# Performance work log

Hardware: AMD Instinct MI355X
Metric: run time of the kernel (lower is better)

Reference implementation:

```python
import jax, jax.numpy as jnp
import numpy as np

MARGIN = 0.2  # init margin
B, D = 4096, 512


def _pairwise_dist(x):
    # torch.cdist(x, x, p=2): Euclidean distance via Gram matrix
    sq = jnp.sum(x * x, axis=-1)                      # [B]
    gram = x @ x.T                                    # [B, B]
    d2 = jnp.maximum(sq[:, None] + sq[None, :] - 2.0 * gram, 0.0)
    safe = jnp.where(d2 > 0, d2, 1.0)                 # grad-safe sqrt at 0
    return jnp.where(d2 > 0, jnp.sqrt(safe), 0.0)


def setup_inputs() -> dict:
    key = jax.random.key(0)
    k1, k2, k3 = jax.random.split(key, 3)
    anchor = jax.random.normal(k1, (B, D), dtype=jnp.float32)
    positive = jax.random.normal(k2, (B, D), dtype=jnp.float32)
    labels = jax.random.randint(k3, (B,), 0, 64)
    return {"anchor": anchor, "positive": positive, "labels": labels}


def reference(anchor, positive, labels):
    d_ap = jnp.sum((anchor - positive) ** 2, axis=-1)          # [B] squared dist
    pd = _pairwise_dist(anchor)                                 # [B, B] euclidean
    diff_label = labels[None, :] != labels[:, None]             # [B, B]
    inf = jnp.float32(jnp.inf)
    # negatives farther than the positive (note: pd is euclidean, d_ap squared,
    # exactly as in the original code)
    cand = jnp.where(diff_label & (pd > d_ap[:, None]), pd, inf)
    min_larger = jnp.min(cand, axis=1)
    # fallback: min over all different-label negatives
    fallback = jnp.min(jnp.where(diff_label, pd, inf), axis=1)
    d_an = jnp.where(jnp.isfinite(min_larger), min_larger, fallback)
    loss = jnp.maximum(d_ap - d_an + MARGIN, 0.0)
    return jnp.mean(loss)
```

## Files before the change

kernel.cpp:

```cpp
#include <hip/hip_runtime.h>
#include <hip/hip_bf16.h>
#include <cstdint>
#include <cstddef>

constexpr int BN = 4096;
constexpr int DN = 512;
constexpr int NT = BN / 128;
constexpr int NBLK = NT * (NT + 1) / 2;
constexpr float MARGIN = 0.2f;
constexpr uint32_t INF_U = 0x7f800000u;

typedef __attribute__((ext_vector_type(8))) short short8;
typedef __attribute__((ext_vector_type(4))) float float4v;

__global__ __launch_bounds__(256) void prep_kernel(
    const float* __restrict__ anchor,
    const float* __restrict__ positive,
    const int* __restrict__ labels,
    uint16_t* __restrict__ Abf,
    float4* __restrict__ meta,
    uint32_t* __restrict__ min_all,
    uint32_t* __restrict__ min_larger,
    uint32_t* __restrict__ done_count)
{
    const int tid  = threadIdx.x;
    const int wave = tid >> 6;
    const int lane = tid & 63;
    const int row  = blockIdx.x * 4 + wave;

    if (blockIdx.x == 0 && tid == 0) *done_count = 0;

    const float4* arow = (const float4*)(anchor   + (size_t)row * DN);
    const float4* prow = (const float4*)(positive + (size_t)row * DN);

    float4 av0 = arow[lane * 2 + 0], av1 = arow[lane * 2 + 1];
    float4 pv0 = prow[lane * 2 + 0], pv1 = prow[lane * 2 + 1];

    float a[8] = {av0.x, av0.y, av0.z, av0.w, av1.x, av1.y, av1.z, av1.w};
    float p[8] = {pv0.x, pv0.y, pv0.z, pv0.w, pv1.x, pv1.y, pv1.z, pv1.w};

    float s = 0.f, d = 0.f;
    union { uint16_t u[8]; uint4 v; } pk;
    #pragma unroll
    for (int i = 0; i < 8; ++i) {
        s += a[i] * a[i];
        float dx = a[i] - p[i];
        d += dx * dx;
        uint32_t ub = __float_as_uint(a[i]);
        pk.u[i] = (uint16_t)((ub + 0x7fffu + ((ub >> 16) & 1u)) >> 16);
    }

    ((uint4*)(Abf + (size_t)row * DN))[lane] = pk.v;

    #pragma unroll
    for (int off = 32; off; off >>= 1) {
        s += __shfl_xor(s, off);
        d += __shfl_xor(d, off);
    }
    if (lane == 0) {
        meta[row] = (float4){s, d, d * d, __uint_as_float((uint32_t)labels[row])};
        min_all[row]    = INF_U;
        min_larger[row] = INF_U;
    }
}

__global__ __launch_bounds__(256, 2) void gram_kernel(
    const uint16_t* __restrict__ Abf,
    const float4* __restrict__ meta,
    uint32_t* __restrict__ min_all,
    uint32_t* __restrict__ min_larger,
    uint32_t* __restrict__ done_count,
    float* __restrict__ out)
{
    __shared__ uint16_t Abuf[128 * 128];
    __shared__ uint16_t Bbuf[128 * 128];

    int t = blockIdx.x, bi = 0, rem = NT;
    while (t >= rem) { t -= rem; ++bi; --rem; }
    const int bj = bi + t;
    const bool offdiag = (bi != bj);
    const int rowBase = bi * 128;
    const int colBase = bj * 128;

    const int tid  = threadIdx.x;
    const int wave = tid >> 6;
    const int lane = tid & 63;
    const int wi   = wave >> 1;
    const int wj   = wave & 1;
    const int quad = lane >> 4;
    const int l15  = lane & 15;

    int sr[8], sc[8], sp[8];
    #pragma unroll
    for (int i = 0; i < 8; ++i) {
        int l = tid + i * 256;
        sr[i] = l >> 4; sc[i] = l & 15; sp[i] = sc[i] ^ (sr[i] & 15);
    }

    float4v acc[4][4];
    #pragma unroll
    for (int i = 0; i < 4; ++i)
        #pragma unroll
        for (int j = 0; j < 4; ++j)
            acc[i][j] = (float4v){0.f, 0.f, 0.f, 0.f};

    for (int kt = 0; kt < DN / 128; ++kt) {
        const int k0 = kt * 128;
        __syncthreads();
        {
            uint4 sA[8], sB[8];
            #pragma unroll
            for (int i = 0; i < 8; ++i)
                sA[i] = *(const uint4*)(Abf + (size_t)(rowBase + sr[i]) * DN + k0 + sc[i] * 8);
            #pragma unroll
            for (int i = 0; i < 8; ++i)
                sB[i] = *(const uint4*)(Abf + (size_t)(colBase + sr[i]) * DN + k0 + sc[i] * 8);
            #pragma unroll
            for (int i = 0; i < 8; ++i)
                *(uint4*)(Abuf + sr[i] * 128 + sp[i] * 8) = sA[i];
            #pragma unroll
            for (int i = 0; i < 8; ++i)
                *(uint4*)(Bbuf + sr[i] * 128 + sp[i] * 8) = sB[i];
        }
        __syncthreads();

        #pragma unroll
        for (int kk = 0; kk < 4; ++kk) {
            short8 af[4], bfr[4];
            #pragma unroll
            for (int mi = 0; mi < 4; ++mi) {
                int r = wi * 64 + mi * 16 + l15;
                int p = (kk * 4 + quad) ^ (r & 15);
                af[mi] = *(const short8*)(Abuf + r * 128 + p * 8);
            }
            #pragma unroll
            for (int mj = 0; mj < 4; ++mj) {
                int r = wj * 64 + mj * 16 + l15;
                int p = (kk * 4 + quad) ^ (r & 15);
                bfr[mj] = *(const short8*)(Bbuf + r * 128 + p * 8);
            }
            #pragma unroll
            for (int mi = 0; mi < 4; ++mi)
                #pragma unroll
                for (int mj = 0; mj < 4; ++mj)
                    acc[mi][mj] = __builtin_amdgcn_mfma_f32_16x16x32_bf16(
                        af[mi], bfr[mj], acc[mi][mj], 0, 0, 0);
        }
    }

    const float INFF = __uint_as_float(INF_U);
    float4 mj_meta[4];
    #pragma unroll
    for (int mj = 0; mj < 4; ++mj)
        mj_meta[mj] = meta[colBase + wj * 64 + mj * 16 + l15];

    float cAll[4], cLarger[4];
    #pragma unroll
    for (int mj = 0; mj < 4; ++mj) { cAll[mj] = INFF; cLarger[mj] = INFF; }

    #pragma unroll
    for (int mi = 0; mi < 4; ++mi) {
        #pragma unroll
        for (int r = 0; r < 4; ++r) {
            int row = rowBase + wi * 64 + mi * 16 + quad * 4 + r;
            float4 mim = meta[row];
            uint32_t li = __float_as_uint(mim.w);
            float mAll = INFF, mLarger = INFF;
            #pragma unroll
            for (int mj = 0; mj < 4; ++mj) {
                float d2 = mim.x + mj_meta[mj].x - 2.0f * acc[mi][mj][r];
                d2 = d2 > 0.f ? d2 : 0.f;
                if (__float_as_uint(mj_meta[mj].w) != li) {
                    mAll = fminf(mAll, d2);
                    if (d2 > mim.z) mLarger = fminf(mLarger, d2);
                    if (offdiag) {
                        cAll[mj] = fminf(cAll[mj], d2);
                        if (d2 > mj_meta[mj].z) cLarger[mj] = fminf(cLarger[mj], d2);
                    }
                }
            }
            #pragma unroll
            for (int off = 1; off < 16; off <<= 1) {
                mAll    = fminf(mAll,    __shfl_xor(mAll, off));
                mLarger = fminf(mLarger, __shfl_xor(mLarger, off));
            }
            if (l15 == 0) {
                atomicMin(&min_all[row],    __float_as_uint(mAll));
                atomicMin(&min_larger[row], __float_as_uint(mLarger));
            }
        }
    }
    if (offdiag) {
        #pragma unroll
        for (int mj = 0; mj < 4; ++mj) {
            float a0 = cAll[mj], l0 = cLarger[mj];
            a0 = fminf(a0, __shfl_xor(a0, 16)); l0 = fminf(l0, __shfl_xor(l0, 16));
            a0 = fminf(a0, __shfl_xor(a0, 32)); l0 = fminf(l0, __shfl_xor(l0, 32));
            if (quad == 0) {
                int col = colBase + wj * 64 + mj * 16 + l15;
                atomicMin(&min_all[col],    __float_as_uint(a0));
                atomicMin(&min_larger[col], __float_as_uint(l0));
            }
        }
    }

    __shared__ bool isLast;
    __syncthreads();
    if (tid == 0) {
        __threadfence();
        isLast = (atomicAdd(done_count, 1u) == NBLK - 1);
    }
    __syncthreads();
    if (isLast) {
        __threadfence();
        float s = 0.f;
        for (int i = tid; i < BN; i += 256) {
            uint32_t mlu = __hip_atomic_load(&min_larger[i], __ATOMIC_RELAXED, __HIP_MEMORY_SCOPE_AGENT);
            uint32_t mau = __hip_atomic_load(&min_all[i],    __ATOMIC_RELAXED, __HIP_MEMORY_SCOPE_AGENT);
            float dan2 = (mlu != INF_U) ? __uint_as_float(mlu) : __uint_as_float(mau);
            float l = meta[i].y - sqrtf(dan2) + MARGIN;
            s += l > 0.f ? l : 0.f;
        }
        #pragma unroll
        for (int off = 32; off; off >>= 1) s += __shfl_xor(s, off);
        __shared__ float wsum[4];
        if ((tid & 63) == 0) wsum[tid >> 6] = s;
        __syncthreads();
        if (tid == 0) out[0] = (wsum[0] + wsum[1] + wsum[2] + wsum[3]) * (1.0f / BN);
    }
}

extern "C" void kernel_launch(void* const* d_in, const int* in_sizes, int n_in,
                              void* d_out, int out_size, void* d_ws, size_t ws_size,
                              hipStream_t stream) {
    const float* anchor   = (const float*)d_in[0];
    const float* positive = (const float*)d_in[1];
    const int*   labels   = (const int*)d_in[2];
    float* out = (float*)d_out;

    uint8_t* ws = (uint8_t*)d_ws;
    uint16_t* Abf        = (uint16_t*)ws;
    float4*   meta       = (float4*)(ws + (size_t)BN * DN * 2);
    uint32_t* min_all    = (uint32_t*)(meta + BN);
    uint32_t* min_larger = min_all + BN;
    uint32_t* done_count = min_larger + BN;

    prep_kernel<<<BN / 4, 256, 0, stream>>>(anchor, positive, labels, Abf, meta,
                                            min_all, min_larger, done_count);
    gram_kernel<<<NBLK, 256, 0, stream>>>(Abf, meta, min_all, min_larger, done_count, out);
}
```

Before: 119.5 us.

## Replace global atomicMin reductions with per-tile partial buffers and finalize kernel

```diff
diff --git a/kernel.cpp b/kernel.cpp
--- a/kernel.cpp
+++ b/kernel.cpp
@@ -19,8 +19,6 @@
     const int* __restrict__ labels,
     uint16_t* __restrict__ Abf,
     float4* __restrict__ meta,
-    uint32_t* __restrict__ min_all,
-    uint32_t* __restrict__ min_larger,
     uint32_t* __restrict__ done_count)
 {
     const int tid  = threadIdx.x;
@@ -57,20 +55,15 @@
         s += __shfl_xor(s, off);
         d += __shfl_xor(d, off);
     }
-    if (lane == 0) {
+    if (lane == 0)
         meta[row] = (float4){s, d, d * d, __uint_as_float((uint32_t)labels[row])};
-        min_all[row]    = INF_U;
-        min_larger[row] = INF_U;
-    }
 }
 
 __global__ __launch_bounds__(256, 2) void gram_kernel(
     const uint16_t* __restrict__ Abf,
     const float4* __restrict__ meta,
-    uint32_t* __restrict__ min_all,
-    uint32_t* __restrict__ min_larger,
-    uint32_t* __restrict__ done_count,
-    float* __restrict__ out)
+    uint32_t* __restrict__ partial_all,
+    uint32_t* __restrict__ partial_larger)
 {
     __shared__ uint16_t Abuf[128 * 128];
     __shared__ uint16_t Bbuf[128 * 128];
@@ -185,8 +178,8 @@
                 mLarger = fminf(mLarger, __shfl_xor(mLarger, off));
             }
             if (l15 == 0) {
-                atomicMin(&min_all[row],    __float_as_uint(mAll));
-                atomicMin(&min_larger[row], __float_as_uint(mLarger));
+                partial_all   [(size_t)row * NT + bj] = __float_as_uint(mAll);
+                partial_larger[(size_t)row * NT + bj] = __float_as_uint(mLarger);
             }
         }
     }
@@ -198,35 +191,59 @@
             a0 = fminf(a0, __shfl_xor(a0, 32)); l0 = fminf(l0, __shfl_xor(l0, 32));
             if (quad == 0) {
                 int col = colBase + wj * 64 + mj * 16 + l15;
-                atomicMin(&min_all[col],    __float_as_uint(a0));
-                atomicMin(&min_larger[col], __float_as_uint(l0));
-            }
-        }
-    }
+                partial_all   [(size_t)col * NT + bi] = __float_as_uint(a0);
+                partial_larger[(size_t)col * NT + bi] = __float_as_uint(l0);
+            }
+        }
+    }
+}
+
+__global__ __launch_bounds__(256) void finalize_kernel(
+    const float4* __restrict__ meta,
+    const uint32_t* __restrict__ partial_all,
+    const uint32_t* __restrict__ partial_larger,
+    float* __restrict__ psum,
+    uint32_t* __restrict__ done_count,
+    float* __restrict__ out)
+{
+    const int tid = threadIdx.x;
+    const int row = blockIdx.x * 256 + tid;
+    const float INFF = __uint_as_float(INF_U);
+
+    float mAll = INFF, mLarger = INFF;
+    const uint4* pa = (const uint4*)(partial_all    + (size_t)row * NT);
+    const uint4* pl = (const uint4*)(partial_larger + (size_t)row * NT);
+    #pragma unroll
+    for (int i = 0; i < 8; ++i) {
+        uint4 a = pa[i], l = pl[i];
+        mAll = fminf(mAll, fminf(fminf(__uint_as_float(a.x), __uint_as_float(a.y)),
+                                 fminf(__uint_as_float(a.z), __uint_as_float(a.w))));
+        mLarger = fminf(mLarger, fminf(fminf(__uint_as_float(l.x), __uint_as_float(l.y)),
+                                       fminf(__uint_as_float(l.z), __uint_as_float(l.w))));
+    }
+    float dan2 = (__float_as_uint(mLarger) != INF_U) ? mLarger : mAll;
+    float lv = meta[row].y - sqrtf(dan2) + MARGIN;
+    float s = lv > 0.f ? lv : 0.f;
+
+    #pragma unroll
+    for (int off = 32; off; off >>= 1) s += __shfl_xor(s, off);
+    __shared__ float wsum[4];
+    if ((tid & 63) == 0) wsum[tid >> 6] = s;
+    __syncthreads();
 
     __shared__ bool isLast;
+    if (tid == 0) {
+        psum[blockIdx.x] = wsum[0] + wsum[1] + wsum[2] + wsum[3];
+        __threadfence();
+        isLast = (atomicAdd(done_count, 1u) == 16 - 1);
+    }
     __syncthreads();
-    if (tid == 0) {
+    if (isLast && tid == 0) {
         __threadfence();
-        isLast = (atomicAdd(done_count, 1u) == NBLK - 1);
-    }
-    __syncthreads();
-    if (isLast) {
-        __threadfence();
-        float s = 0.f;
-        for (int i = tid; i < BN; i += 256) {
-            uint32_t mlu = __hip_atomic_load(&min_larger[i], __ATOMIC_RELAXED, __HIP_MEMORY_SCOPE_AGENT);
-            uint32_t mau = __hip_atomic_load(&min_all[i],    __ATOMIC_RELAXED, __HIP_MEMORY_SCOPE_AGENT);
-            float dan2 = (mlu != INF_U) ? __uint_as_float(mlu) : __uint_as_float(mau);
-            float l = meta[i].y - sqrtf(dan2) + MARGIN;
-            s += l > 0.f ? l : 0.f;
-        }
-        #pragma unroll
-        for (int off = 32; off; off >>= 1) s += __shfl_xor(s, off);
-        __shared__ float wsum[4];
-        if ((tid & 63) == 0) wsum[tid >> 6] = s;
-        __syncthreads();
-        if (tid == 0) out[0] = (wsum[0] + wsum[1] + wsum[2] + wsum[3]) * (1.0f / BN);
+        float tot = 0.f;
+        for (int b = 0; b < 16; ++b)
+            tot += __hip_atomic_load(&psum[b], __ATOMIC_RELAXED, __HIP_MEMORY_SCOPE_AGENT);
+        out[0] = tot * (1.0f / BN);
     }
 }
 
@@ -239,13 +256,15 @@
     float* out = (float*)d_out;
 
     uint8_t* ws = (uint8_t*)d_ws;
-    uint16_t* Abf        = (uint16_t*)ws;
-    float4*   meta       = (float4*)(ws + (size_t)BN * DN * 2);
-    uint32_t* min_all    = (uint32_t*)(meta + BN);
-    uint32_t* min_larger = min_all + BN;
-    uint32_t* done_count = min_larger + BN;
-
-    prep_kernel<<<BN / 4, 256, 0, stream>>>(anchor, positive, labels, Abf, meta,
-                                            min_all, min_larger, done_count);
-    gram_kernel<<<NBLK, 256, 0, stream>>>(Abf, meta, min_all, min_larger, done_count, out);
-}
+    uint16_t* Abf            = (uint16_t*)ws;
+    float4*   meta           = (float4*)(ws + (size_t)BN * DN * 2);
+    uint32_t* partial_all    = (uint32_t*)(meta + BN);
+    uint32_t* partial_larger = partial_all + (size_t)BN * NT;
+    float*    psum           = (float*)(partial_larger + (size_t)BN * NT);
+    uint32_t* done_count     = (uint32_t*)(psum + 16);
+
+    prep_kernel<<<BN / 4, 256, 0, stream>>>(anchor, positive, labels, Abf, meta, done_count);
+    gram_kernel<<<NBLK, 256, 0, stream>>>(Abf, meta, partial_all, partial_larger);
+    finalize_kernel<<<16, 256, 0, stream>>>(meta, partial_all, partial_larger,
+                                            psum, done_count, out);
+}
```

Result: faster. 110.3 us (-7.7%).
